# Performance work log

Hardware: AMD Instinct MI355X
Metric: run time of the kernel (lower is better)

Reference implementation:

```python
import jax, jax.numpy as jnp
import numpy as np

HEADS, DIM_HEAD, NEIGHBORS = 8, 64, 64
REL_DIST_SCALE, REL_DIST_CUTOFF, THETA, EPS = 100.0, 5000.0, 10000.0, 1e-8


def _rotate_half(x):
    # interleaved pairs: (x0,x1),(x2,x3),... -> (-x1,x0),(-x3,x2),...
    xp = x.reshape(*x.shape[:-1], -1, 2)
    a, b = xp[..., 0], xp[..., 1]
    return jnp.stack((-b, a), axis=-1).reshape(x.shape)


def _apply_rotary(t, freqs):
    return t * jnp.cos(freqs) + _rotate_half(t) * jnp.sin(freqs)


def _gelu(x):
    return jax.nn.gelu(x, approximate=False)  # torch nn.GELU default = exact erf


def setup_inputs() -> dict:
    key = jax.random.key(0)
    ks = jax.random.split(key, 12)
    b, n, d, e = 2, 2048, 256, 16
    h, dh = HEADS, DIM_HEAD
    inner = h * dh
    std = 0.02
    return {
        "feats": jax.random.normal(ks[0], (b, n, d), jnp.float32),
        "coors": jax.random.normal(ks[1], (b, n, 3), jnp.float32),
        "edges": jax.random.normal(ks[2], (b, n, n, e), jnp.float32),
        "W_qkv": jax.random.normal(ks[3], (d, inner * 3), jnp.float32) * std,
        "W_out": jax.random.normal(ks[4], (inner, d), jnp.float32) * std,
        "b_out": jnp.zeros((d,), jnp.float32),
        "W_e1": jax.random.normal(ks[5], (h + e, 2 * (h + e)), jnp.float32) * std,
        "b_e1": jnp.zeros((2 * (h + e),), jnp.float32),
        "W_e2": jax.random.normal(ks[6], (2 * (h + e), h), jnp.float32) * std,
        "b_e2": jnp.zeros((h,), jnp.float32),
        "W_c": jax.random.normal(ks[7], (h, h), jnp.float32) * std,
        "b_c": jnp.zeros((h,), jnp.float32),
        "W_g": jax.random.normal(ks[8], (h, h), jnp.float32) * std,
        "b_g": jnp.zeros((h,), jnp.float32),
        "coors_combine": jax.random.normal(ks[9], (h,), jnp.float32),
        "coors_scale": jnp.ones((1,), jnp.float32),
    }


def reference(feats, coors, edges, W_qkv, W_out, b_out, W_e1, b_e1, W_e2, b_e2,
              W_c, b_c, W_g, b_g, coors_combine, coors_scale):
    b, n, d = feats.shape
    h, dh, nn_k = HEADS, DIM_HEAD, NEIGHBORS

    # pairwise relative coordinates / distances (O(n^2) irregular part)
    rel_coors = coors[:, :, None, :] - coors[:, None, :, :]            # b n n 3
    rel_dist = jnp.linalg.norm(rel_coors, axis=-1)                      # b n n

    # topk nearest neighbors (largest=False -> top_k of negated distances)
    _, nbhd_idx = jax.lax.top_k(-rel_dist, nn_k)                        # b n nn

    qkv = feats @ W_qkv                                                 # b n 3*h*dh
    q, k, v = jnp.split(qkv, 3, axis=-1)
    q = q.reshape(b, n, h, dh).transpose(0, 2, 1, 3)                    # b h n dh
    k = k.reshape(b, n, h, dh).transpose(0, 2, 1, 3)
    v = v.reshape(b, n, h, dh).transpose(0, 2, 1, 3)

    # batched_index_select gathers
    k = jax.vmap(lambda kb, ib: kb[:, ib])(k, nbhd_idx)                 # b h n nn dh
    v = jax.vmap(lambda vb, ib: vb[:, ib])(v, nbhd_idx)                 # b h n nn dh
    rel_dist_nb = jnp.take_along_axis(rel_dist, nbhd_idx, axis=2)       # b n nn
    rel_coors_nb = jnp.take_along_axis(rel_coors, nbhd_idx[..., None], axis=2)  # b n nn 3
    edges_nb = jnp.take_along_axis(edges, nbhd_idx[..., None], axis=2)  # b n nn e

    # rotary on relative distances; q's freqs are zeros -> identity rotation (skipped)
    inv_freq = 1.0 / (THETA ** (jnp.arange(0, dh, 2, dtype=jnp.float32) / dh))
    t = jnp.minimum(rel_dist_nb * REL_DIST_SCALE, REL_DIST_CUTOFF)
    freqs = jnp.repeat(t[..., None] * inv_freq, 2, axis=-1)[:, None]    # b 1 n nn dh
    k = _apply_rotary(k, freqs)
    v = _apply_rotary(v, freqs)

    # edges provided -> no 1/sqrt(dh) scale, then edge MLP
    qk = jnp.einsum('bhid,bhijd->bhij', q, k)                           # b h i j
    qk = jnp.transpose(qk, (0, 2, 3, 1))                                # b i j h
    x = jnp.concatenate([qk, edges_nb], axis=-1)                        # b i j (h+e)
    qk = _gelu(x @ W_e1 + b_e1) @ W_e2 + b_e2                           # b i j h

    # coordinate attention branch (coors_mlp = GELU + Linear when edges exist)
    coor_weights = _gelu(qk) @ W_c + b_c                                # b i j h
    coor_attn = jax.nn.softmax(coor_weights, axis=2)                    # softmax over j
    gate = jnp.tanh(qk @ W_g + b_g)                                     # b i j h

    nrm = jnp.linalg.norm(rel_coors_nb, axis=-1, keepdims=True)
    rel_normed = rel_coors_nb / jnp.maximum(nrm, EPS) * coors_scale     # b i j 3

    rel_out = jnp.einsum('bijh,bijc->bich', coor_attn * gate, rel_normed)
    coors_delta = jnp.einsum('bich,h->bic', rel_out, coors_combine)     # b n 3

    # feature attention branch
    attn = jax.nn.softmax(jnp.transpose(qk, (0, 3, 1, 2)), axis=-1)     # b h i j
    out = jnp.einsum('bhij,bhijd->bhid', attn, v)
    out = out.transpose(0, 2, 1, 3).reshape(b, n, h * dh)
    node_out = out @ W_out + b_out                                      # b n d
    return node_out, coors_delta
```

## Files before the change

kernel.cpp:

```cpp
#include <hip/hip_runtime.h>
#include <hip/hip_fp16.h>
#include <math.h>

#define NPTS 2048
#define NB 64
#define H 8
#define DH 64
#define INNER 512

__device__ __forceinline__ float gelu_exact(float x) {
  return 0.5f * x * (1.0f + erff(x * 0.7071067811865475f));
}

__device__ __forceinline__ unsigned int pack_cs(float c, float s) {
  __half2 h = __floats2half2_rn(c, s);
  return *reinterpret_cast<unsigned int*>(&h);
}
__device__ __forceinline__ float2 unpack_cs(unsigned int u) {
  __half2 h = *reinterpret_cast<__half2*>(&u);
  return __half22float2(h);
}

__global__ __launch_bounds__(256) void topk_kernel(const float* __restrict__ coors,
                                                   int* __restrict__ nbhd) {
  const int row = blockIdx.x;
  const int b = row >> 11;
  const int tid = threadIdx.x;
  const int lane = tid & 63;
  const int wv = tid >> 6;
  __shared__ unsigned long long list[4][64];

  const float* cb = coors + (size_t)b * NPTS * 3;
  const float cx = coors[(size_t)row * 3 + 0];
  const float cy = coors[(size_t)row * 3 + 1];
  const float cz = coors[(size_t)row * 3 + 2];

  unsigned long long keys[8];
#pragma unroll
  for (int s = 0; s < 8; ++s) {
    const int j = (wv << 9) + (s << 6) + lane;
    const float dx = cx - cb[j * 3 + 0];
    const float dy = cy - cb[j * 3 + 1];
    const float dz = cz - cb[j * 3 + 2];
    const float d = sqrtf(dx * dx + dy * dy + dz * dz);
    keys[s] = (((unsigned long long)__float_as_uint(d)) << 32) | (unsigned long long)j;
  }

#define CAS(a, b)                                                   \
  {                                                                 \
    unsigned long long lo = keys[a] < keys[b] ? keys[a] : keys[b];  \
    unsigned long long hi = keys[a] < keys[b] ? keys[b] : keys[a];  \
    keys[a] = lo; keys[b] = hi;                                     \
  }
  CAS(0, 1) CAS(2, 3) CAS(4, 5) CAS(6, 7)
  CAS(0, 2) CAS(1, 3) CAS(4, 6) CAS(5, 7)
  CAS(1, 2) CAS(5, 6)
  CAS(0, 4) CAS(1, 5) CAS(2, 6) CAS(3, 7)
  CAS(2, 4) CAS(3, 5)
  CAS(1, 2) CAS(3, 4) CAS(5, 6)
#undef CAS

  for (int r = 0; r < NB; ++r) {
    unsigned long long w = keys[0];
#pragma unroll
    for (int off = 32; off > 0; off >>= 1) {
      unsigned long long o = __shfl_xor(w, off, 64);
      w = o < w ? o : w;
    }
    const bool win = (keys[0] == w);
#pragma unroll
    for (int i = 0; i < 7; ++i) keys[i] = win ? keys[i + 1] : keys[i];
    keys[7] = win ? ~0ull : keys[7];
    if (lane == (r & 63)) list[wv][r] = w;
  }
  __syncthreads();

  {
    const unsigned long long c = list[wv][lane];
    int rank = lane;
#pragma unroll
    for (int o = 1; o < 4; ++o) {
      const unsigned long long* L = list[(wv + o) & 3];
      int base = 0;
#pragma unroll
      for (int sz = 32; sz > 0; sz >>= 1)
        if (L[base + sz - 1] < c) base += sz;
      rank += base;
    }
    if (rank < NB) nbhd[(size_t)row * NB + rank] = (int)(c & 0xffffffffull);
  }
}

__global__ __launch_bounds__(256) void gemm_tiled(const float* __restrict__ A,
                                                  const float* __restrict__ B,
                                                  const float* __restrict__ bias,
                                                  float* __restrict__ C,
                                                  int M, int N, int K) {
  __shared__ float As[16][68];
  __shared__ float Bs[16][68];
  const int tid = threadIdx.x;
  const int tx = tid & 15;
  const int ty = tid >> 4;
  const int n0 = blockIdx.x << 6;
  const int m0 = blockIdx.y << 6;
  const int la_m = tid >> 2;
  const int la_k = (tid & 3) << 2;
  const int lb_k = tid >> 4;
  const int lb_n = (tid & 15) << 2;
  float acc[4][4] = {{0.f}};
  for (int kk = 0; kk < K; kk += 16) {
    const float4 a4 = *(const float4*)(A + (size_t)(m0 + la_m) * K + kk + la_k);
    const float4 b4 = *(const float4*)(B + (size_t)(kk + lb_k) * N + n0 + lb_n);
    As[la_k + 0][la_m] = a4.x;
    As[la_k + 1][la_m] = a4.y;
    As[la_k + 2][la_m] = a4.z;
    As[la_k + 3][la_m] = a4.w;
    *(float4*)(&Bs[lb_k][lb_n]) = b4;
    __syncthreads();
#pragma unroll
    for (int k = 0; k < 16; ++k) {
      const float4 av = *(const float4*)(&As[k][ty << 2]);
      const float4 bv = *(const float4*)(&Bs[k][tx << 2]);
      acc[0][0] += av.x * bv.x; acc[0][1] += av.x * bv.y; acc[0][2] += av.x * bv.z; acc[0][3] += av.x * bv.w;
      acc[1][0] += av.y * bv.x; acc[1][1] += av.y * bv.y; acc[1][2] += av.y * bv.z; acc[1][3] += av.y * bv.w;
      acc[2][0] += av.z * bv.x; acc[2][1] += av.z * bv.y; acc[2][2] += av.z * bv.z; acc[2][3] += av.z * bv.w;
      acc[3][0] += av.w * bv.x; acc[3][1] += av.w * bv.y; acc[3][2] += av.w * bv.z; acc[3][3] += av.w * bv.w;
    }
    __syncthreads();
  }
#pragma unroll
  for (int r = 0; r < 4; ++r) {
#pragma unroll
    for (int c = 0; c < 4; ++c) {
      const int n = n0 + (tx << 2) + c;
      float v = acc[r][c];
      if (bias) v += bias[n];
      C[(size_t)(m0 + (ty << 2) + r) * N + n] = v;
    }
  }
}

__global__ __launch_bounds__(256, 4) void attn_kernel(
    const float* __restrict__ qkv, const float* __restrict__ coors,
    const float* __restrict__ edges, const int* __restrict__ nbhd,
    const float* __restrict__ W_e1, const float* __restrict__ b_e1,
    const float* __restrict__ W_e2, const float* __restrict__ b_e2,
    const float* __restrict__ W_c, const float* __restrict__ b_c,
    const float* __restrict__ W_g, const float* __restrict__ b_g,
    const float* __restrict__ coors_combine, const float* __restrict__ coors_scale,
    float* __restrict__ attn_out, float* __restrict__ coors_out) {
  __shared__ float q_s[H][68];
  __shared__ unsigned int cs_s[NB][33];
  __shared__ float qk_s[NB][9];
  __shared__ float qk2_s[NB][9];
  __shared__ float attn_s[NB][9];
  __shared__ float edg_s[NB][17];
  __shared__ float rel_s[NB][4];
  __shared__ float dist_s[NB];
  __shared__ int idx_s[NB];
  __shared__ float We1[24 * 48];
  __shared__ float We2[48 * 9];
  __shared__ float be1[48];
  __shared__ float be2[H], bcs[H], bgs[H], ccs[H];
  __shared__ float Wcs[H * H], Wgs[H * H];
  __shared__ float invf[32];
  __shared__ float credx[4][3];

  const int row = blockIdx.x;
  const int b = row >> 11;
  const int tid = threadIdx.x;
  const size_t qbase = (size_t)row * 1536;

  {
    int t0 = tid;
    q_s[t0 >> 6][t0 & 63] = qkv[qbase + t0];
    int t1 = tid + 256;
    q_s[t1 >> 6][t1 & 63] = qkv[qbase + t1];
  }
  for (int t = tid; t < 24 * 48; t += 256) We1[t] = W_e1[t];
  for (int t = tid; t < 48 * H; t += 256) We2[(t >> 3) * 9 + (t & 7)] = W_e2[t];
  if (tid < 48) be1[tid] = b_e1[tid];
  if (tid < H) { be2[tid] = b_e2[tid]; bcs[tid] = b_c[tid]; bgs[tid] = b_g[tid]; ccs[tid] = coors_combine[tid]; }
  if (tid < H * H) { Wcs[tid] = W_c[tid]; Wgs[tid] = W_g[tid]; }
  if (tid < 32) invf[tid] = expf(-(float)tid * 0.28782313662425575f);
  if (tid < NB) {
    const int jj = nbhd[(size_t)row * NB + tid];
    idx_s[tid] = jj;
    const float csc = coors_scale[0];
    const float dx = coors[(size_t)row * 3 + 0] - coors[((size_t)b * NPTS + jj) * 3 + 0];
    const float dy = coors[(size_t)row * 3 + 1] - coors[((size_t)b * NPTS + jj) * 3 + 1];
    const float dz = coors[(size_t)row * 3 + 2] - coors[((size_t)b * NPTS + jj) * 3 + 2];
    const float d = sqrtf(dx * dx + dy * dy + dz * dz);
    dist_s[tid] = d;
    const float inv = csc / fmaxf(d, 1e-8f);
    rel_s[tid][0] = dx * inv;
    rel_s[tid][1] = dy * inv;
    rel_s[tid][2] = dz * inv;
  }
  __syncthreads();

#pragma unroll
  for (int s = 0; s < 8; ++s) {
    const int p = tid + (s << 8);
    const int j = p >> 5, m = p & 31;
    const float t = fminf(dist_s[j] * 100.0f, 5000.0f);
    float sv, cv;
    __sincosf(t * invf[m], &sv, &cv);
    cs_s[j][m] = pack_cs(cv, sv);
  }
  {
    const size_t ebase = (size_t)row * NPTS * 16;
#pragma unroll
    for (int s = 0; s < 4; ++s) {
      const int p = tid + (s << 8);
      const int j = p >> 4, e = p & 15;
      edg_s[j][e] = edges[ebase + (size_t)idx_s[j] * 16 + e];
    }
  }
  __syncthreads();

#pragma unroll
  for (int s = 0; s < 2; ++s) {
    const int p = tid + (s << 8);
    const int j = p >> 3, h = p & 7;
    const float* krow = qkv + ((size_t)b * NPTS + idx_s[j]) * 1536 + INNER + h * DH;
    float acc = 0.f;
#pragma unroll
    for (int m4 = 0; m4 < 16; ++m4) {
      const float4 kv = *(const float4*)(krow + (m4 << 2));
      const float4 qv = *(const float4*)(&q_s[h][m4 << 2]);
      const int m = m4 << 1;
      const float2 c0 = unpack_cs(cs_s[j][m]);
      const float2 c1 = unpack_cs(cs_s[j][m + 1]);
      acc += qv.x * (kv.x * c0.x - kv.y * c0.y) + qv.y * (kv.y * c0.x + kv.x * c0.y) +
             qv.z * (kv.z * c1.x - kv.w * c1.y) + qv.w * (kv.w * c1.x + kv.z * c1.y);
    }
    qk_s[j][h] = acc;
  }
  __syncthreads();

  {
    const int j = tid >> 2, part = tid & 3;
    float hv[12];
#pragma unroll
    for (int l = 0; l < 12; ++l) {
      const int hh = part * 12 + l;
      float a = be1[hh];
#pragma unroll
      for (int r = 0; r < 8; ++r) a += qk_s[j][r] * We1[r * 48 + hh];
#pragma unroll
      for (int r = 0; r < 16; ++r) a += edg_s[j][r] * We1[(8 + r) * 48 + hh];
      hv[l] = gelu_exact(a);
    }
    float p8[8];
#pragma unroll
    for (int h = 0; h < 8; ++h) {
      float a = 0.f;
#pragma unroll
      for (int l = 0; l < 12; ++l) a += hv[l] * We2[(part * 12 + l) * 9 + h];
      a += __shfl_xor(a, 1, 64);
      a += __shfl_xor(a, 2, 64);
      p8[h] = a + be2[h];
    }
    qk2_s[j][(part << 1) + 0] = p8[(part << 1) + 0];
    qk2_s[j][(part << 1) + 1] = p8[(part << 1) + 1];
  }
  __syncthreads();

  {
    const int lane = tid & 63;
    const int wv = tid >> 6;
    float qv[8], ge[8];
#pragma unroll
    for (int r = 0; r < 8; ++r) { qv[r] = qk2_s[lane][r]; ge[r] = gelu_exact(qv[r]); }
    float wpart = 0.f;
#pragma unroll
    for (int hh = 0; hh < 2; ++hh) {
      const int h = (wv << 1) + hh;
      float y = qv[h];
      float my = y;
#pragma unroll
      for (int off = 32; off > 0; off >>= 1) my = fmaxf(my, __shfl_xor(my, off, 64));
      const float e2 = __expf(y - my);
      float s2 = e2;
#pragma unroll
      for (int off = 32; off > 0; off >>= 1) s2 += __shfl_xor(s2, off, 64);
      attn_s[lane][h] = e2 / s2;
      float cwv = bcs[h], gt = bgs[h];
#pragma unroll
      for (int r = 0; r < 8; ++r) {
        cwv += ge[r] * Wcs[r * 8 + h];
        gt += qv[r] * Wgs[r * 8 + h];
      }
      gt = tanhf(gt);
      float mx = cwv;
#pragma unroll
      for (int off = 32; off > 0; off >>= 1) mx = fmaxf(mx, __shfl_xor(mx, off, 64));
      const float e = __expf(cwv - mx);
      float sm = e;
#pragma unroll
      for (int off = 32; off > 0; off >>= 1) sm += __shfl_xor(sm, off, 64);
      wpart += (e / sm) * gt * ccs[h];
    }
    float px = wpart * rel_s[lane][0];
    float py = wpart * rel_s[lane][1];
    float pz = wpart * rel_s[lane][2];
#pragma unroll
    for (int off = 32; off > 0; off >>= 1) {
      px += __shfl_xor(px, off, 64);
      py += __shfl_xor(py, off, 64);
      pz += __shfl_xor(pz, off, 64);
    }
    if (lane == 0) { credx[wv][0] = px; credx[wv][1] = py; credx[wv][2] = pz; }
  }
  __syncthreads();

  if (tid == 0) {
    coors_out[(size_t)row * 3 + 0] = credx[0][0] + credx[1][0] + credx[2][0] + credx[3][0];
    coors_out[(size_t)row * 3 + 1] = credx[0][1] + credx[1][1] + credx[2][1] + credx[3][1];
    coors_out[(size_t)row * 3 + 2] = credx[0][2] + credx[1][2] + credx[2][2] + credx[3][2];
  }

  {
    const int h = tid >> 5, m = tid & 31;
    const size_t off_v = (size_t)(2 * INNER + h * DH + (m << 1));
    float o0 = 0.f, o1 = 0.f;
#pragma unroll 8
    for (int j = 0; j < NB; ++j) {
      const float2 v = *(const float2*)(qkv + ((size_t)b * NPTS + idx_s[j]) * 1536 + off_v);
      const float2 cs = unpack_cs(cs_s[j][m]);
      const float a = attn_s[j][h];
      o0 += a * (v.x * cs.x - v.y * cs.y);
      o1 += a * (v.y * cs.x + v.x * cs.y);
    }
    *(float2*)(attn_out + (size_t)row * INNER + h * DH + (m << 1)) = make_float2(o0, o1);
  }
}

extern "C" void kernel_launch(void* const* d_in, const int* in_sizes, int n_in,
                              void* d_out, int out_size, void* d_ws, size_t ws_size,
                              hipStream_t stream) {
  const float* feats = (const float*)d_in[0];
  const float* coors = (const float*)d_in[1];
  const float* edges = (const float*)d_in[2];
  const float* W_qkv = (const float*)d_in[3];
  const float* W_out = (const float*)d_in[4];
  const float* b_out = (const float*)d_in[5];
  const float* W_e1 = (const float*)d_in[6];
  const float* b_e1 = (const float*)d_in[7];
  const float* W_e2 = (const float*)d_in[8];
  const float* b_e2 = (const float*)d_in[9];
  const float* W_c = (const float*)d_in[10];
  const float* b_c = (const float*)d_in[11];
  const float* W_g = (const float*)d_in[12];
  const float* b_g = (const float*)d_in[13];
  const float* cc = (const float*)d_in[14];
  const float* cscale = (const float*)d_in[15];

  float* out = (float*)d_out;
  float* qkv = (float*)d_ws;
  float* attn_out = qkv + (size_t)4096 * 1536;
  int* nbhd = (int*)(attn_out + (size_t)4096 * 512);

  gemm_tiled<<<dim3(24, 64), 256, 0, stream>>>(feats, W_qkv, nullptr, qkv, 4096, 1536, 256);
  topk_kernel<<<4096, 256, 0, stream>>>(coors, nbhd);
  attn_kernel<<<4096, 256, 0, stream>>>(qkv, coors, edges, nbhd,
                                        W_e1, b_e1, W_e2, b_e2, W_c, b_c, W_g, b_g,
                                        cc, cscale, attn_out, out + (size_t)4096 * 256);
  gemm_tiled<<<dim3(4, 64), 256, 0, stream>>>(attn_out, W_out, b_out, out, 4096, 256, 512);
}
```

Measured before the change: 1.002 ms.

## Fuse top-k into attention kernel and gather K/V from half-precision copy

The separate top-k neighbor kernel is merged into the attention kernel, so neighbor indices and distances stay in shared memory instead of going through a global buffer and a second launch. The QKV GEMM epilogue also writes an fp16 copy of K and V, which the attention kernel gathers instead of the fp32 rows, halving gather bytes. The per-lane inverse frequency table is replaced by an inline exp. The changes lower precision of K/V, and the fused kernel gets longer, which may affect occupancy.

```diff
diff --git a/kernel.cpp b/kernel.cpp
--- a/kernel.cpp
+++ b/kernel.cpp
@@ -20,81 +20,16 @@
   __half2 h = *reinterpret_cast<__half2*>(&u);
   return __half22float2(h);
 }
-
-__global__ __launch_bounds__(256) void topk_kernel(const float* __restrict__ coors,
-                                                   int* __restrict__ nbhd) {
-  const int row = blockIdx.x;
-  const int b = row >> 11;
-  const int tid = threadIdx.x;
-  const int lane = tid & 63;
-  const int wv = tid >> 6;
-  __shared__ unsigned long long list[4][64];
-
-  const float* cb = coors + (size_t)b * NPTS * 3;
-  const float cx = coors[(size_t)row * 3 + 0];
-  const float cy = coors[(size_t)row * 3 + 1];
-  const float cz = coors[(size_t)row * 3 + 2];
-
-  unsigned long long keys[8];
-#pragma unroll
-  for (int s = 0; s < 8; ++s) {
-    const int j = (wv << 9) + (s << 6) + lane;
-    const float dx = cx - cb[j * 3 + 0];
-    const float dy = cy - cb[j * 3 + 1];
-    const float dz = cz - cb[j * 3 + 2];
-    const float d = sqrtf(dx * dx + dy * dy + dz * dz);
-    keys[s] = (((unsigned long long)__float_as_uint(d)) << 32) | (unsigned long long)j;
-  }
-
-#define CAS(a, b)                                                   \
-  {                                                                 \
-    unsigned long long lo = keys[a] < keys[b] ? keys[a] : keys[b];  \
-    unsigned long long hi = keys[a] < keys[b] ? keys[b] : keys[a];  \
-    keys[a] = lo; keys[b] = hi;                                     \
-  }
-  CAS(0, 1) CAS(2, 3) CAS(4, 5) CAS(6, 7)
-  CAS(0, 2) CAS(1, 3) CAS(4, 6) CAS(5, 7)
-  CAS(1, 2) CAS(5, 6)
-  CAS(0, 4) CAS(1, 5) CAS(2, 6) CAS(3, 7)
-  CAS(2, 4) CAS(3, 5)
-  CAS(1, 2) CAS(3, 4) CAS(5, 6)
-#undef CAS
-
-  for (int r = 0; r < NB; ++r) {
-    unsigned long long w = keys[0];
-#pragma unroll
-    for (int off = 32; off > 0; off >>= 1) {
-      unsigned long long o = __shfl_xor(w, off, 64);
-      w = o < w ? o : w;
-    }
-    const bool win = (keys[0] == w);
-#pragma unroll
-    for (int i = 0; i < 7; ++i) keys[i] = win ? keys[i + 1] : keys[i];
-    keys[7] = win ? ~0ull : keys[7];
-    if (lane == (r & 63)) list[wv][r] = w;
-  }
-  __syncthreads();
-
-  {
-    const unsigned long long c = list[wv][lane];
-    int rank = lane;
-#pragma unroll
-    for (int o = 1; o < 4; ++o) {
-      const unsigned long long* L = list[(wv + o) & 3];
-      int base = 0;
-#pragma unroll
-      for (int sz = 32; sz > 0; sz >>= 1)
-        if (L[base + sz - 1] < c) base += sz;
-      rank += base;
-    }
-    if (rank < NB) nbhd[(size_t)row * NB + rank] = (int)(c & 0xffffffffull);
-  }
+__device__ __forceinline__ float2 h2_to_f2(unsigned int u) {
+  __half2 h = *reinterpret_cast<__half2*>(&u);
+  return __half22float2(h);
 }
 
 __global__ __launch_bounds__(256) void gemm_tiled(const float* __restrict__ A,
                                                   const float* __restrict__ B,
                                                   const float* __restrict__ bias,
                                                   float* __restrict__ C,
+                                                  __half* __restrict__ kvh,
                                                   int M, int N, int K) {
   __shared__ float As[16][68];
   __shared__ float Bs[16][68];
@@ -128,21 +63,32 @@
     }
     __syncthreads();
   }
+  const bool do_kv = (kvh != nullptr) && (n0 >= 512);
 #pragma unroll
   for (int r = 0; r < 4; ++r) {
+    const int m = m0 + (ty << 2) + r;
+    const int nb = n0 + (tx << 2);
+    float v[4];
 #pragma unroll
     for (int c = 0; c < 4; ++c) {
-      const int n = n0 + (tx << 2) + c;
-      float v = acc[r][c];
-      if (bias) v += bias[n];
-      C[(size_t)(m0 + (ty << 2) + r) * N + n] = v;
-    }
-  }
-}
-
-__global__ __launch_bounds__(256, 4) void attn_kernel(
-    const float* __restrict__ qkv, const float* __restrict__ coors,
-    const float* __restrict__ edges, const int* __restrict__ nbhd,
+      v[c] = acc[r][c];
+      if (bias) v[c] += bias[nb + c];
+      C[(size_t)m * N + nb + c] = v[c];
+    }
+    if (do_kv) {
+      __half2 h01 = __floats2half2_rn(v[0], v[1]);
+      __half2 h23 = __floats2half2_rn(v[2], v[3]);
+      uint2 pk;
+      pk.x = *reinterpret_cast<unsigned int*>(&h01);
+      pk.y = *reinterpret_cast<unsigned int*>(&h23);
+      *(uint2*)(kvh + (size_t)m * 1024 + (nb - 512)) = pk;
+    }
+  }
+}
+
+__global__ __launch_bounds__(256, 4) void fused_attn(
+    const float* __restrict__ qkv, const __half* __restrict__ kvh,
+    const float* __restrict__ coors, const float* __restrict__ edges,
     const float* __restrict__ W_e1, const float* __restrict__ b_e1,
     const float* __restrict__ W_e2, const float* __restrict__ b_e2,
     const float* __restrict__ W_c, const float* __restrict__ b_c,
@@ -163,12 +109,14 @@
   __shared__ float be1[48];
   __shared__ float be2[H], bcs[H], bgs[H], ccs[H];
   __shared__ float Wcs[H * H], Wgs[H * H];
-  __shared__ float invf[32];
   __shared__ float credx[4][3];
+  __shared__ unsigned long long list[4][64];
 
   const int row = blockIdx.x;
   const int b = row >> 11;
   const int tid = threadIdx.x;
+  const int lane = tid & 63;
+  const int wv = tid >> 6;
   const size_t qbase = (size_t)row * 1536;
 
   {
@@ -182,40 +130,99 @@
   if (tid < 48) be1[tid] = b_e1[tid];
   if (tid < H) { be2[tid] = b_e2[tid]; bcs[tid] = b_c[tid]; bgs[tid] = b_g[tid]; ccs[tid] = coors_combine[tid]; }
   if (tid < H * H) { Wcs[tid] = W_c[tid]; Wgs[tid] = W_g[tid]; }
-  if (tid < 32) invf[tid] = expf(-(float)tid * 0.28782313662425575f);
+
+  const float* cb = coors + (size_t)b * NPTS * 3;
+  const float cx = coors[(size_t)row * 3 + 0];
+  const float cy = coors[(size_t)row * 3 + 1];
+  const float cz = coors[(size_t)row * 3 + 2];
+  {
+    unsigned long long keys[8];
+#pragma unroll
+    for (int s = 0; s < 8; ++s) {
+      const int j = (wv << 9) + (s << 6) + lane;
+      const float dx = cx - cb[j * 3 + 0];
+      const float dy = cy - cb[j * 3 + 1];
+      const float dz = cz - cb[j * 3 + 2];
+      const float d = sqrtf(dx * dx + dy * dy + dz * dz);
+      keys[s] = (((unsigned long long)__float_as_uint(d)) << 32) | (unsigned long long)j;
+    }
+#define CAS(a, b)                                                   \
+    {                                                               \
+      unsigned long long lo = keys[a] < keys[b] ? keys[a] : keys[b];\
+      unsigned long long hi = keys[a] < keys[b] ? keys[b] : keys[a];\
+      keys[a] = lo; keys[b] = hi;                                   \
+    }
+    CAS(0, 1) CAS(2, 3) CAS(4, 5) CAS(6, 7)
+    CAS(0, 2) CAS(1, 3) CAS(4, 6) CAS(5, 7)
+    CAS(1, 2) CAS(5, 6)
+    CAS(0, 4) CAS(1, 5) CAS(2, 6) CAS(3, 7)
+    CAS(2, 4) CAS(3, 5)
+    CAS(1, 2) CAS(3, 4) CAS(5, 6)
+#undef CAS
+    for (int r = 0; r < NB; ++r) {
+      unsigned long long w = keys[0];
+#pragma unroll
+      for (int off = 32; off > 0; off >>= 1) {
+        unsigned long long o = __shfl_xor(w, off, 64);
+        w = o < w ? o : w;
+      }
+      const bool win = (keys[0] == w);
+#pragma unroll
+      for (int i = 0; i < 7; ++i) keys[i] = win ? keys[i + 1] : keys[i];
+      keys[7] = win ? ~0ull : keys[7];
+      if (lane == (r & 63)) list[wv][r] = w;
+    }
+  }
+  __syncthreads();
+
+  {
+    const unsigned long long c = list[wv][lane];
+    int rank = lane;
+#pragma unroll
+    for (int o = 1; o < 4; ++o) {
+      const unsigned long long* L = list[(wv + o) & 3];
+      int base = 0;
+#pragma unroll
+      for (int sz = 32; sz > 0; sz >>= 1)
+        if (L[base + sz - 1] < c) base += sz;
+      rank += base;
+    }
+    if (rank < NB) {
+      idx_s[rank] = (int)(c & 0xffffffffull);
+      dist_s[rank] = __uint_as_float((unsigned int)(c >> 32));
+    }
+  }
+  __syncthreads();
+
+  {
+    const size_t ebase = (size_t)row * NPTS * 16;
+#pragma unroll
+    for (int s = 0; s < 4; ++s) {
+      const int p = tid + (s << 8);
+      const int j = p >> 4, e = p & 15;
+      edg_s[j][e] = edges[ebase + (size_t)idx_s[j] * 16 + e];
+    }
+  }
   if (tid < NB) {
-    const int jj = nbhd[(size_t)row * NB + tid];
-    idx_s[tid] = jj;
+    const int jj = idx_s[tid];
     const float csc = coors_scale[0];
-    const float dx = coors[(size_t)row * 3 + 0] - coors[((size_t)b * NPTS + jj) * 3 + 0];
-    const float dy = coors[(size_t)row * 3 + 1] - coors[((size_t)b * NPTS + jj) * 3 + 1];
-    const float dz = coors[(size_t)row * 3 + 2] - coors[((size_t)b * NPTS + jj) * 3 + 2];
-    const float d = sqrtf(dx * dx + dy * dy + dz * dz);
-    dist_s[tid] = d;
-    const float inv = csc / fmaxf(d, 1e-8f);
+    const float dx = cx - cb[jj * 3 + 0];
+    const float dy = cy - cb[jj * 3 + 1];
+    const float dz = cz - cb[jj * 3 + 2];
+    const float inv = csc / fmaxf(dist_s[tid], 1e-8f);
     rel_s[tid][0] = dx * inv;
     rel_s[tid][1] = dy * inv;
     rel_s[tid][2] = dz * inv;
   }
-  __syncthreads();
-
 #pragma unroll
   for (int s = 0; s < 8; ++s) {
     const int p = tid + (s << 8);
     const int j = p >> 5, m = p & 31;
     const float t = fminf(dist_s[j] * 100.0f, 5000.0f);
+    const float invf = __expf(-(float)m * 0.28782313662425575f);
     float sv, cv;
-    __sincosf(t * invf[m], &sv, &cv);
+    __sincosf(t * invf, &sv, &cv);
     cs_s[j][m] = pack_cs(cv, sv);
-  }
-  {
-    const size_t ebase = (size_t)row * NPTS * 16;
-#pragma unroll
-    for (int s = 0; s < 4; ++s) {
-      const int p = tid + (s << 8);
-      const int j = p >> 4, e = p & 15;
-      edg_s[j][e] = edges[ebase + (size_t)idx_s[j] * 16 + e];
-    }
   }
   __syncthreads();
 
@@ -223,17 +230,19 @@
   for (int s = 0; s < 2; ++s) {
     const int p = tid + (s << 8);
     const int j = p >> 3, h = p & 7;
-    const float* krow = qkv + ((size_t)b * NPTS + idx_s[j]) * 1536 + INNER + h * DH;
+    const uint2* krow = (const uint2*)(kvh + ((size_t)b * NPTS + idx_s[j]) * 1024 + h * DH);
     float acc = 0.f;
 #pragma unroll
     for (int m4 = 0; m4 < 16; ++m4) {
-      const float4 kv = *(const float4*)(krow + (m4 << 2));
+      const uint2 ku = krow[m4];
+      const float2 k01 = h2_to_f2(ku.x);
+      const float2 k23 = h2_to_f2(ku.y);
       const float4 qv = *(const float4*)(&q_s[h][m4 << 2]);
       const int m = m4 << 1;
       const float2 c0 = unpack_cs(cs_s[j][m]);
       const float2 c1 = unpack_cs(cs_s[j][m + 1]);
-      acc += qv.x * (kv.x * c0.x - kv.y * c0.y) + qv.y * (kv.y * c0.x + kv.x * c0.y) +
-             qv.z * (kv.z * c1.x - kv.w * c1.y) + qv.w * (kv.w * c1.x + kv.z * c1.y);
+      acc += qv.x * (k01.x * c0.x - k01.y * c0.y) + qv.y * (k01.y * c0.x + k01.x * c0.y) +
+             qv.z * (k23.x * c1.x - k23.y * c1.y) + qv.w * (k23.y * c1.x + k23.x * c1.y);
     }
     qk_s[j][h] = acc;
   }
@@ -268,8 +277,6 @@
   __syncthreads();
 
   {
-    const int lane = tid & 63;
-    const int wv = tid >> 6;
     float qv[8], ge[8];
 #pragma unroll
     for (int r = 0; r < 8; ++r) { qv[r] = qk2_s[lane][r]; ge[r] = gelu_exact(qv[r]); }
@@ -323,11 +330,12 @@
 
   {
     const int h = tid >> 5, m = tid & 31;
-    const size_t off_v = (size_t)(2 * INNER + h * DH + (m << 1));
+    const size_t off_v = (size_t)(512 + h * DH + (m << 1));
     float o0 = 0.f, o1 = 0.f;
 #pragma unroll 8
     for (int j = 0; j < NB; ++j) {
-      const float2 v = *(const float2*)(qkv + ((size_t)b * NPTS + idx_s[j]) * 1536 + off_v);
+      const unsigned int vu = *(const unsigned int*)(kvh + ((size_t)b * NPTS + idx_s[j]) * 1024 + off_v);
+      const float2 v = h2_to_f2(vu);
       const float2 cs = unpack_cs(cs_s[j][m]);
       const float a = attn_s[j][h];
       o0 += a * (v.x * cs.x - v.y * cs.y);
@@ -360,12 +368,11 @@
   float* out = (float*)d_out;
   float* qkv = (float*)d_ws;
   float* attn_out = qkv + (size_t)4096 * 1536;
-  int* nbhd = (int*)(attn_out + (size_t)4096 * 512);
-
-  gemm_tiled<<<dim3(24, 64), 256, 0, stream>>>(feats, W_qkv, nullptr, qkv, 4096, 1536, 256);
-  topk_kernel<<<4096, 256, 0, stream>>>(coors, nbhd);
-  attn_kernel<<<4096, 256, 0, stream>>>(qkv, coors, edges, nbhd,
-                                        W_e1, b_e1, W_e2, b_e2, W_c, b_c, W_g, b_g,
-                                        cc, cscale, attn_out, out + (size_t)4096 * 256);
-  gemm_tiled<<<dim3(4, 64), 256, 0, stream>>>(attn_out, W_out, b_out, out, 4096, 256, 512);
-}
+  __half* kvh = (__half*)(attn_out + (size_t)4096 * 512);
+
+  gemm_tiled<<<dim3(24, 64), 256, 0, stream>>>(feats, W_qkv, nullptr, qkv, kvh, 4096, 1536, 256);
+  fused_attn<<<4096, 256, 0, stream>>>(qkv, kvh, coors, edges,
+                                       W_e1, b_e1, W_e2, b_e2, W_c, b_c, W_g, b_g,
+                                       cc, cscale, attn_out, out + (size_t)4096 * 256);
+  gemm_tiled<<<dim3(4, 64), 256, 0, stream>>>(attn_out, W_out, b_out, out, nullptr, 4096, 256, 512);
+}
```

Result: faster. 911.6 us (-9.0%).
